# Kernel optimization log

Measured on AMD Instinct MI355X. Metric: run time of the kernel, lower is better.

Reference implementation:

```python
import jax, jax.numpy as jnp
import numpy as np

LOW_THRESH, HIGH_THRESH = 0.1, 0.2   # kornia canny defaults
HYST_ITERS = 10                      # fixed-point hysteresis iterations (fixed for jit)


def _gaussian_kernel5(sigma=1.0):
    x = jnp.arange(5, dtype=jnp.float32) - 2.0
    g = jnp.exp(-0.5 * (x / sigma) ** 2)
    g = g / g.sum()
    return jnp.outer(g, g)  # [5,5]


def _conv2d(x, k):
    # x: [B,1,H,W]; k: [kh,kw]; reflect pad + VALID conv == SAME with reflect border
    kh, kw = k.shape
    xp = jnp.pad(x, ((0, 0), (0, 0), (kh // 2, kh // 2), (kw // 2, kw // 2)), mode="reflect")
    return jax.lax.conv_general_dilated(
        xp, k[None, None], (1, 1), "VALID",
        dimension_numbers=("NCHW", "OIHW", "NCHW"))


def _shift(x, dy, dx):
    # value of neighbor at (i+dy, j+dx), zero-padded border; x: [B,1,H,W]
    H, W = x.shape[2], x.shape[3]
    xp = jnp.pad(x, ((0, 0), (0, 0), (1, 1), (1, 1)))
    return xp[:, :, 1 + dy:1 + dy + H, 1 + dx:1 + dx + W]


def _canny_edges(img):
    # img: [B,3,H,W] in [0,1] -> binary edge map [B,1,H,W]
    gray = 0.299 * img[:, :1] + 0.587 * img[:, 1:2] + 0.114 * img[:, 2:3]
    blur = _conv2d(gray, _gaussian_kernel5())
    sobel_x = jnp.array([[-1., 0., 1.], [-2., 0., 2.], [-1., 0., 1.]], jnp.float32)
    gx = _conv2d(blur, sobel_x)
    gy = _conv2d(blur, sobel_x.T)
    mag = jnp.sqrt(gx * gx + gy * gy + 1e-12)
    ang = jnp.arctan2(gy, gx)

    # non-maximum suppression: quantize gradient direction to 4 bins (0/45/90/135 deg)
    b = jnp.mod(jnp.round(ang / (jnp.pi / 4.0)), 4).astype(jnp.int32)  # [B,1,H,W]
    n_pos = jnp.stack([_shift(mag, 0, 1), _shift(mag, 1, 1),
                       _shift(mag, 1, 0), _shift(mag, 1, -1)], axis=0)  # [4,B,1,H,W]
    n_neg = jnp.stack([_shift(mag, 0, -1), _shift(mag, -1, -1),
                       _shift(mag, -1, 0), _shift(mag, -1, 1)], axis=0)
    n1 = jnp.take_along_axis(n_pos, b[None], axis=0)[0]
    n2 = jnp.take_along_axis(n_neg, b[None], axis=0)[0]
    nms = jnp.where((mag >= n1) & (mag >= n2), mag, 0.0)

    # double threshold: strong=1.0, weak=0.5
    edges = jnp.where(nms >= HIGH_THRESH, 1.0,
                      jnp.where(nms >= LOW_THRESH, 0.5, 0.0))

    # hysteresis: weak pixels with a strong 8-neighbor become strong (iterated)
    def body(_, e):
        strong = (e == 1.0).astype(e.dtype)
        nb = jax.lax.reduce_window(strong, 0.0, jax.lax.max,
                                   (1, 1, 3, 3), (1, 1, 1, 1), "SAME")
        promoted = (e == 0.5) & (nb > 0.5)
        return jnp.where(promoted, 1.0, e)

    edges = jax.lax.fori_loop(0, HYST_ITERS, body, edges)
    return (edges == 1.0).astype(jnp.float32)


def setup_inputs() -> dict:
    key = jax.random.key(0)
    k1, k2 = jax.random.split(key)
    shape = (16, 3, 512, 512)
    return {"y_hat": jax.random.uniform(k1, shape, jnp.float32),
            "y": jax.random.uniform(k2, shape, jnp.float32)}


def reference(y_hat, y):
    y_hat_edges = _canny_edges(y_hat)
    y_edges = _canny_edges(y)
    return jnp.mean(jnp.abs(y_hat_edges - y_edges))  # F.l1_loss, mean reduction
```

## Files before the change

kernel.cpp:

```cpp
#include <hip/hip_runtime.h>
#include <math.h>

#define H 512
#define W 512
#define IMG (H*W)
#define NIMG 32
#define NSTRIP 10
#define SW 56
#define RB 32
#define NBAND 16

typedef unsigned long long u64;

__device__ __forceinline__ int reflect_idx(int i, int n) {
    if (i < 0) i = -i;
    if (i >= n) i = 2 * n - 2 - i;
    return i;
}

__device__ __forceinline__ float bperm_f(int addr, float v) {
    return __int_as_float(__builtin_amdgcn_ds_bpermute(addr, __float_as_int(v)));
}

#define S0 0.05448868454964294f
#define S1 0.35317871110251920f
#define S2 0.94551131545035710f
#define S3 1.29364257779496160f
#define A1 0.05448868454964294f
#define A2 0.24420134200323332f
#define A3 0.34813126234460456f

__global__ __launch_bounds__(256) void k_edges(const float* __restrict__ yhat,
                                               const float* __restrict__ yy,
                                               u64* __restrict__ strongP,
                                               u64* __restrict__ weakP) {
    const int wid = blockIdx.x * 4 + (threadIdx.x >> 6);
    const int lane = threadIdx.x & 63;
    const int n = wid / (NSTRIP * NBAND);
    const int rem = wid - n * (NSTRIP * NBAND);
    const int s = rem >> 4;
    const int band = rem & 15;
    const int y0 = band * RB;
    const float* src = (n < 16) ? (yhat + (size_t)n * 3 * IMG)
                                : (yy + (size_t)(n - 16) * 3 * IMG);

    const int c = s * SW - 4 + lane;
    const int cx = reflect_idx(c, W);
    const bool colok = ((unsigned)c < (unsigned)W);
    const u64 omask = (s == 9) ? 0xFFull : 0x00FFFFFFFFFFFFFFull;

    const int aM3 = ((lane - 3) << 2), aM2 = ((lane - 2) << 2), aM1 = ((lane - 1) << 2);
    const int aP1 = ((lane + 1) << 2), aP2 = ((lane + 2) << 2), aP3 = ((lane + 3) << 2);

    float hx[7], hy[7];
    float mPrev = 0.f, mPrevL = 0.f, mPrevR = 0.f;
    float mCur = 0.f, mCurL = 0.f, mCurR = 0.f;
    int dCur = 0, dNew = 0;

    u64 outBase = ((size_t)n * NSTRIP + s) * H;

    for (int i = 0; i < RB + 8; i++) {
#pragma unroll
        for (int j = 0; j < 6; j++) { hx[j] = hx[j + 1]; hy[j] = hy[j + 1]; }
        {
            int gr = reflect_idx(y0 - 4 + i, H);
            const float* p = src + (size_t)gr * W + cx;
            float g = 0.299f * p[0] + 0.587f * p[IMG] + 0.114f * p[2 * IMG];
            float gm1 = bperm_f(aM1, g), gp1 = bperm_f(aP1, g);
            float gm2 = bperm_f(aM2, g), gp2 = bperm_f(aP2, g);
            float gm3 = bperm_f(aM3, g), gp3 = bperm_f(aP3, g);
            hx[6] = A3 * (gp1 - gm1) + A2 * (gp2 - gm2) + A1 * (gp3 - gm3);
            hy[6] = S3 * g + S2 * (gp1 + gm1) + S1 * (gp2 + gm2) + S0 * (gp3 + gm3);
        }

        float mNew = 0.f, mNewL = 0.f, mNewR = 0.f;
        if (i >= 6) {
            float gx = S3 * hx[3] + S2 * (hx[4] + hx[2])
                     + S1 * (hx[5] + hx[1]) + S0 * (hx[6] + hx[0]);
            float gy = A3 * (hy[4] - hy[2]) + A2 * (hy[5] - hy[1])
                     + A1 * (hy[6] - hy[0]);
            int mr = y0 - 7 + i;
            bool ok = colok && ((unsigned)mr < (unsigned)H);
            mNew = ok ? (gx * gx + gy * gy + 1e-12f) : 0.f;
            mNewL = bperm_f(aM1, mNew);
            mNewR = bperm_f(aP1, mNew);
            float ax = fabsf(gx), ay = fabsf(gy);
            dNew = (ay <= 0.4142135623730951f * ax) ? 0
                 : (ay >= 2.414213562373095f * ax) ? 2
                 : (((gx > 0.f) == (gy > 0.f)) ? 1 : 3);
        }

        if (i >= 8) {
            float n1 = (dCur == 0) ? mCurR : (dCur == 1) ? mNewR
                     : (dCur == 2) ? mNew : mNewL;
            float n2 = (dCur == 0) ? mCurL : (dCur == 1) ? mPrevL
                     : (dCur == 2) ? mPrev : mPrevR;
            bool okn = (mCur >= n1) && (mCur >= n2);
            u64 bs = __ballot(okn && (mCur >= 0.04f));
            u64 bw = __ballot(okn && (mCur >= 0.01f));
            if (lane == 0) {
                int t = y0 - 8 + i;
                strongP[outBase + t] = (bs >> 4) & omask;
                weakP[outBase + t] = (bw >> 4) & omask;
            }
        }

        if (i >= 6) {
            mPrev = mCur; mPrevL = mCurL; mPrevR = mCurR;
            mCur = mNew; mCurL = mNewL; mCurR = mNewR;
            dCur = dNew;
        }
    }
}

__device__ __forceinline__ u64 ldw10(const u64* p, int img, int y, int q, bool ok) {
    return (ok && q >= 0 && q < NSTRIP) ? p[((size_t)img * NSTRIP + q) * H + y] : 0ULL;
}

__global__ __launch_bounds__(256) void k_hyst(const u64* __restrict__ strongP,
                                              const u64* __restrict__ weakP,
                                              unsigned int* __restrict__ partials) {
    __shared__ unsigned int part[4];
    const int wy = threadIdx.x >> 6;
    const int wave = blockIdx.x * 4 + wy;
    const int lane = threadIdx.x & 63;
    const int tile = wave & 255;
    const int pair = wave >> 8;
    const int tx0 = (tile & 15) * 32;
    const int ty0 = (tile >> 4) * 32;

    const int y = ty0 - 10 + lane;
    const bool rowok = (lane < 52) && (y >= 0) && (y < H);
    const int yc = rowok ? y : 0;

    const int x = tx0 - 10;
    const int q0 = (x < 0) ? -1 : (x / 56);
    const int r = x - 56 * q0;
    const int sh1 = 56 - r;
    const bool need3 = (r > 48);
    const int sh2 = 112 - r;

    const int imgA = pair, imgB = pair + 16;
    u64 sA, wA, sB, wB;
    {
        u64 w0, w1, w2;
        w0 = ldw10(strongP, imgA, yc, q0, rowok);
        w1 = ldw10(strongP, imgA, yc, q0 + 1, rowok);
        w2 = need3 ? ldw10(strongP, imgA, yc, q0 + 2, rowok) : 0ULL;
        sA = (w0 >> r) | (w1 << sh1) | (need3 ? (w2 << sh2) : 0ULL);
        w0 = ldw10(weakP, imgA, yc, q0, rowok);
        w1 = ldw10(weakP, imgA, yc, q0 + 1, rowok);
        w2 = need3 ? ldw10(weakP, imgA, yc, q0 + 2, rowok) : 0ULL;
        wA = (w0 >> r) | (w1 << sh1) | (need3 ? (w2 << sh2) : 0ULL);
        w0 = ldw10(strongP, imgB, yc, q0, rowok);
        w1 = ldw10(strongP, imgB, yc, q0 + 1, rowok);
        w2 = need3 ? ldw10(strongP, imgB, yc, q0 + 2, rowok) : 0ULL;
        sB = (w0 >> r) | (w1 << sh1) | (need3 ? (w2 << sh2) : 0ULL);
        w0 = ldw10(weakP, imgB, yc, q0, rowok);
        w1 = ldw10(weakP, imgB, yc, q0 + 1, rowok);
        w2 = need3 ? ldw10(weakP, imgB, yc, q0 + 2, rowok) : 0ULL;
        wB = (w0 >> r) | (w1 << sh1) | (need3 ? (w2 << sh2) : 0ULL);
    }

#pragma unroll
    for (int it = 0; it < 10; it++) {
        u64 up = __shfl_up(sA, 1), dn = __shfl_down(sA, 1);
        u64 t = up | sA | dn;
        sA |= (t | (t << 1) | (t >> 1)) & wA;
        up = __shfl_up(sB, 1); dn = __shfl_down(sB, 1);
        t = up | sB | dn;
        sB |= (t | (t << 1) | (t >> 1)) & wB;
    }

    unsigned int cgt = 0;
    if (lane >= 10 && lane < 42) {
        const u64 mask = ((1ULL << 42) - (1ULL << 10));
        cgt = (unsigned int)__popcll((sA ^ sB) & mask);
    }
#pragma unroll
    for (int off = 32; off > 0; off >>= 1) cgt += __shfl_down(cgt, off);
    if (lane == 0) part[wy] = cgt;
    __syncthreads();
    if (threadIdx.x == 0)
        partials[blockIdx.x] = part[0] + part[1] + part[2] + part[3];
}

__global__ __launch_bounds__(256) void k_final(const unsigned int* __restrict__ partials,
                                               float* __restrict__ out) {
    __shared__ unsigned int part[4];
    unsigned int c = 0;
    for (int i = threadIdx.x; i < 1024; i += 256) c += partials[i];
#pragma unroll
    for (int off = 32; off > 0; off >>= 1) c += __shfl_down(c, off);
    const int lane = threadIdx.x & 63;
    const int wy = threadIdx.x >> 6;
    if (lane == 0) part[wy] = c;
    __syncthreads();
    if (threadIdx.x == 0)
        out[0] = (float)(part[0] + part[1] + part[2] + part[3]) * (1.0f / 4194304.0f);
}

extern "C" void kernel_launch(void* const* d_in, const int* in_sizes, int n_in,
                              void* d_out, int out_size, void* d_ws, size_t ws_size,
                              hipStream_t stream) {
    const float* yhat = (const float*)d_in[0];
    const float* yy = (const float*)d_in[1];

    u64* strongP = (u64*)d_ws;
    u64* weakP = strongP + (size_t)NIMG * NSTRIP * H;
    unsigned int* partials = (unsigned int*)(weakP + (size_t)NIMG * NSTRIP * H);

    k_edges<<<1280, 256, 0, stream>>>(yhat, yy, strongP, weakP);

    k_hyst<<<1024, 256, 0, stream>>>(strongP, weakP, partials);
    k_final<<<1, 256, 0, stream>>>(partials, (float*)d_out);
}
```

Before: 146.6 us.

## Split edge kernel into prologue and fully unrolled steady loop with prefetched loads

Shrinks row bands from 32 to 26 rows (20 bands per strip, 1600 blocks) so more waves are in flight. The row loop is split into an 8-iteration prologue and a fully unrolled steady-state loop with no per-iteration branches, and each next row's RGB values are loaded one iteration ahead to hide global load latency. In exchange, the halo overhead per output row rises with smaller bands, a bounds check on the last band is added, and register pressure grows from unrolling.

```diff
diff --git a/kernel.cpp b/kernel.cpp
--- a/kernel.cpp
+++ b/kernel.cpp
@@ -7,8 +7,8 @@
 #define NIMG 32
 #define NSTRIP 10
 #define SW 56
-#define RB 32
-#define NBAND 16
+#define RB 26
+#define NBAND 20
 
 typedef unsigned long long u64;
 
@@ -38,8 +38,8 @@
     const int lane = threadIdx.x & 63;
     const int n = wid / (NSTRIP * NBAND);
     const int rem = wid - n * (NSTRIP * NBAND);
-    const int s = rem >> 4;
-    const int band = rem & 15;
+    const int s = rem / NBAND;
+    const int band = rem - s * NBAND;
     const int y0 = band * RB;
     const float* src = (n < 16) ? (yhat + (size_t)n * 3 * IMG)
                                 : (yy + (size_t)(n - 16) * 3 * IMG);
@@ -53,27 +53,37 @@
     const int aP1 = ((lane + 1) << 2), aP2 = ((lane + 2) << 2), aP3 = ((lane + 3) << 2);
 
     float hx[7], hy[7];
+#pragma unroll
+    for (int j = 0; j < 7; j++) { hx[j] = 0.f; hy[j] = 0.f; }
     float mPrev = 0.f, mPrevL = 0.f, mPrevR = 0.f;
     float mCur = 0.f, mCurL = 0.f, mCurR = 0.f;
-    int dCur = 0, dNew = 0;
-
-    u64 outBase = ((size_t)n * NSTRIP + s) * H;
-
-    for (int i = 0; i < RB + 8; i++) {
+    int dCur = 0;
+
+    const u64 outBase = ((size_t)n * NSTRIP + s) * H;
+
+    float rN, gN, bN;
+    {
+        int gr = reflect_idx(y0 - 4, H);
+        const float* p = src + (size_t)gr * W + cx;
+        rN = p[0]; gN = p[IMG]; bN = p[2 * IMG];
+    }
+
+#pragma unroll
+    for (int i = 0; i < 8; i++) {
+        float g = 0.299f * rN + 0.587f * gN + 0.114f * bN;
+        {
+            int gr = reflect_idx(y0 - 3 + i, H);
+            const float* p = src + (size_t)gr * W + cx;
+            rN = p[0]; gN = p[IMG]; bN = p[2 * IMG];
+        }
+        float gm1 = bperm_f(aM1, g), gp1 = bperm_f(aP1, g);
+        float gm2 = bperm_f(aM2, g), gp2 = bperm_f(aP2, g);
+        float gm3 = bperm_f(aM3, g), gp3 = bperm_f(aP3, g);
 #pragma unroll
         for (int j = 0; j < 6; j++) { hx[j] = hx[j + 1]; hy[j] = hy[j + 1]; }
-        {
-            int gr = reflect_idx(y0 - 4 + i, H);
-            const float* p = src + (size_t)gr * W + cx;
-            float g = 0.299f * p[0] + 0.587f * p[IMG] + 0.114f * p[2 * IMG];
-            float gm1 = bperm_f(aM1, g), gp1 = bperm_f(aP1, g);
-            float gm2 = bperm_f(aM2, g), gp2 = bperm_f(aP2, g);
-            float gm3 = bperm_f(aM3, g), gp3 = bperm_f(aP3, g);
-            hx[6] = A3 * (gp1 - gm1) + A2 * (gp2 - gm2) + A1 * (gp3 - gm3);
-            hy[6] = S3 * g + S2 * (gp1 + gm1) + S1 * (gp2 + gm2) + S0 * (gp3 + gm3);
-        }
-
-        float mNew = 0.f, mNewL = 0.f, mNewR = 0.f;
+        hx[6] = A3 * (gp1 - gm1) + A2 * (gp2 - gm2) + A1 * (gp3 - gm3);
+        hy[6] = S3 * g + S2 * (gp1 + gm1) + S1 * (gp2 + gm2) + S0 * (gp3 + gm3);
+
         if (i >= 6) {
             float gx = S3 * hx[3] + S2 * (hx[4] + hx[2])
                      + S1 * (hx[5] + hx[1]) + S0 * (hx[6] + hx[0]);
@@ -81,35 +91,66 @@
                      + A1 * (hy[6] - hy[0]);
             int mr = y0 - 7 + i;
             bool ok = colok && ((unsigned)mr < (unsigned)H);
-            mNew = ok ? (gx * gx + gy * gy + 1e-12f) : 0.f;
-            mNewL = bperm_f(aM1, mNew);
-            mNewR = bperm_f(aP1, mNew);
+            float mNew = ok ? (gx * gx + gy * gy + 1e-12f) : 0.f;
+            float mNewL = bperm_f(aM1, mNew);
+            float mNewR = bperm_f(aP1, mNew);
             float ax = fabsf(gx), ay = fabsf(gy);
-            dNew = (ay <= 0.4142135623730951f * ax) ? 0
-                 : (ay >= 2.414213562373095f * ax) ? 2
-                 : (((gx > 0.f) == (gy > 0.f)) ? 1 : 3);
-        }
-
-        if (i >= 8) {
-            float n1 = (dCur == 0) ? mCurR : (dCur == 1) ? mNewR
-                     : (dCur == 2) ? mNew : mNewL;
-            float n2 = (dCur == 0) ? mCurL : (dCur == 1) ? mPrevL
-                     : (dCur == 2) ? mPrev : mPrevR;
-            bool okn = (mCur >= n1) && (mCur >= n2);
-            u64 bs = __ballot(okn && (mCur >= 0.04f));
-            u64 bw = __ballot(okn && (mCur >= 0.01f));
-            if (lane == 0) {
-                int t = y0 - 8 + i;
-                strongP[outBase + t] = (bs >> 4) & omask;
-                weakP[outBase + t] = (bw >> 4) & omask;
-            }
-        }
-
-        if (i >= 6) {
+            int dNew = (ay <= 0.4142135623730951f * ax) ? 0
+                     : (ay >= 2.414213562373095f * ax) ? 2
+                     : (((gx > 0.f) == (gy > 0.f)) ? 1 : 3);
             mPrev = mCur; mPrevL = mCurL; mPrevR = mCurR;
             mCur = mNew; mCurL = mNewL; mCurR = mNewR;
             dCur = dNew;
         }
+    }
+
+#pragma unroll
+    for (int ii = 0; ii < RB; ii++) {
+        const int i = 8 + ii;
+        float g = 0.299f * rN + 0.587f * gN + 0.114f * bN;
+        {
+            int gr = reflect_idx(y0 - 3 + i, H);
+            const float* p = src + (size_t)gr * W + cx;
+            rN = p[0]; gN = p[IMG]; bN = p[2 * IMG];
+        }
+        float gm1 = bperm_f(aM1, g), gp1 = bperm_f(aP1, g);
+        float gm2 = bperm_f(aM2, g), gp2 = bperm_f(aP2, g);
+        float gm3 = bperm_f(aM3, g), gp3 = bperm_f(aP3, g);
+#pragma unroll
+        for (int j = 0; j < 6; j++) { hx[j] = hx[j + 1]; hy[j] = hy[j + 1]; }
+        hx[6] = A3 * (gp1 - gm1) + A2 * (gp2 - gm2) + A1 * (gp3 - gm3);
+        hy[6] = S3 * g + S2 * (gp1 + gm1) + S1 * (gp2 + gm2) + S0 * (gp3 + gm3);
+
+        float gx = S3 * hx[3] + S2 * (hx[4] + hx[2])
+                 + S1 * (hx[5] + hx[1]) + S0 * (hx[6] + hx[0]);
+        float gy = A3 * (hy[4] - hy[2]) + A2 * (hy[5] - hy[1])
+                 + A1 * (hy[6] - hy[0]);
+        int mr = y0 - 7 + i;
+        bool ok = colok && ((unsigned)mr < (unsigned)H);
+        float mNew = ok ? (gx * gx + gy * gy + 1e-12f) : 0.f;
+        float mNewL = bperm_f(aM1, mNew);
+        float mNewR = bperm_f(aP1, mNew);
+        float ax = fabsf(gx), ay = fabsf(gy);
+        int dNew = (ay <= 0.4142135623730951f * ax) ? 0
+                 : (ay >= 2.414213562373095f * ax) ? 2
+                 : (((gx > 0.f) == (gy > 0.f)) ? 1 : 3);
+
+        float n1 = (dCur == 0) ? mCurR : (dCur == 1) ? mNewR
+                 : (dCur == 2) ? mNew : mNewL;
+        float n2 = (dCur == 0) ? mCurL : (dCur == 1) ? mPrevL
+                 : (dCur == 2) ? mPrev : mPrevR;
+        bool okn = (mCur >= n1) && (mCur >= n2);
+        u64 bs = __ballot(okn && (mCur >= 0.04f));
+        u64 bw = __ballot(okn && (mCur >= 0.01f));
+        int t = y0 + ii;
+        if (lane == 0 && t < H) {
+            strongP[outBase + t] = (bs >> 4) & omask;
+            weakP[outBase + t] = (bw >> 4) & omask;
+        }
+
+        mPrev = mCur; mPrevL = mCurL; mPrevR = mCurR;
+        mCur = mNew; mCurL = mNewL; mCurR = mNewR;
+        dCur = dNew;
     }
 }
 
@@ -210,7 +251,7 @@
     u64* weakP = strongP + (size_t)NIMG * NSTRIP * H;
     unsigned int* partials = (unsigned int*)(weakP + (size_t)NIMG * NSTRIP * H);
 
-    k_edges<<<1280, 256, 0, stream>>>(yhat, yy, strongP, weakP);
+    k_edges<<<1600, 256, 0, stream>>>(yhat, yy, strongP, weakP);
 
     k_hyst<<<1024, 256, 0, stream>>>(strongP, weakP, partials);
     k_final<<<1, 256, 0, stream>>>(partials, (float*)d_out);
```

Measured after the change: 142.6 us. 1.03x faster.
